# Kernel tuning notes

Measured on AMD Instinct MI355X. Metric: run time of the kernel, lower is better.

Reference implementation:

```python
import jax, jax.numpy as jnp
import numpy as np

EPS = 1e-7
LAMBDA_COORD = 10.0
LAMBDA_NOOBJ = 0.5
LAMBDA_OBJ = 1.0


def setup_inputs() -> dict:
    key = jax.random.key(0)
    k1, k2, k3, k4 = jax.random.split(key, 4)
    B, A, C, G = 64, 3, 20, 76
    predictions = jax.random.normal(k1, (B, A * (5 + C), G, G), dtype=jnp.float32) * 0.5
    txy = jax.random.uniform(k2, (B, A, G, G, 2), dtype=jnp.float32)
    twh = jax.random.normal(k3, (B, A, G, G, 2), dtype=jnp.float32) * 0.3
    tconf = (jax.random.uniform(k4, (B, A, G, G, 1), dtype=jnp.float32) < 0.05).astype(jnp.float32)
    targets = jnp.concatenate([txy, twh, tconf], axis=-1)
    anchors = jnp.array([[1.25, 1.625], [2.0, 3.75], [4.125, 2.875]], dtype=jnp.float32)
    return {"predictions": predictions, "targets": targets, "anchors": anchors}


def _bce(p, t):
    # elementwise binary cross-entropy; p in (0,1) from sigmoid
    return -(t * jnp.log(p) + (1.0 - t) * jnp.log1p(-p))


def _ciou_loss_elem(pb, tb):
    # pb, tb: [..., 4] corner boxes; returns elementwise (1 - ciou)
    x1p, y1p, x2p, y2p = pb[..., 0], pb[..., 1], pb[..., 2], pb[..., 3]
    x1t, y1t, x2t, y2t = tb[..., 0], tb[..., 1], tb[..., 2], tb[..., 3]
    iw = jnp.clip(jnp.minimum(x2p, x2t) - jnp.maximum(x1p, x1t), 0.0)
    ih = jnp.clip(jnp.minimum(y2p, y2t) - jnp.maximum(y1p, y1t), 0.0)
    inter = iw * ih
    area_p = jnp.clip(x2p - x1p, 0.0) * jnp.clip(y2p - y1p, 0.0)
    area_t = jnp.clip(x2t - x1t, 0.0) * jnp.clip(y2t - y1t, 0.0)
    union = area_p + area_t - inter + EPS
    iou = inter / union
    rho2 = ((x1p + x2p - x1t - x2t) * 0.5) ** 2 + ((y1p + y2p - y1t - y2t) * 0.5) ** 2
    en_w = jnp.clip(jnp.maximum(x2p, x2t) - jnp.minimum(x1p, x1t), EPS)
    en_h = jnp.clip(jnp.maximum(y2p, y2t) - jnp.minimum(y1p, y1t), EPS)
    c2 = en_w ** 2 + en_h ** 2
    w_p = jnp.clip(x2p - x1p, EPS); h_p = jnp.clip(y2p - y1p, EPS)
    w_t = jnp.clip(x2t - x1t, EPS); h_t = jnp.clip(y2t - y1t, EPS)
    v = (4.0 / (jnp.pi ** 2)) * (jnp.arctan(w_t / h_t) - jnp.arctan(w_p / h_p)) ** 2
    alpha = jax.lax.stop_gradient(v / (1.0 - iou + v + EPS))
    ciou = iou - rho2 / (c2 + EPS) - alpha * v
    return 1.0 - ciou


def reference(predictions, targets, anchors):
    B, Ch, G, _ = predictions.shape
    A = anchors.shape[0]
    C = Ch // A - 5
    p = predictions.reshape(B, A, 5 + C, G, G).transpose(0, 1, 3, 4, 2)  # [B,A,G,G,5+C]
    pred_xy = jax.nn.sigmoid(p[..., :2])
    pred_wh = p[..., 2:4]
    pred_conf = jax.nn.sigmoid(p[..., 4])
    pred_cls = jax.nn.sigmoid(p[..., 5:])
    obj = targets[..., 4] > 0          # [B,A,G,G]
    n_obj = jnp.sum(obj.astype(jnp.float32))
    n_noobj = jnp.sum((~obj).astype(jnp.float32))
    gy, gx = jnp.meshgrid(jnp.arange(G, dtype=jnp.float32), jnp.arange(G, dtype=jnp.float32), indexing='ij')
    inv_g = 1.0 / G
    aw = anchors[:, 0][None, :, None, None] * inv_g
    ah = anchors[:, 1][None, :, None, None] * inv_g
    # predicted corner boxes
    pcx = (gx + pred_xy[..., 0]) * inv_g
    pcy = (gy + pred_xy[..., 1]) * inv_g
    pw = jnp.exp(pred_wh[..., 0]) * aw
    ph = jnp.exp(pred_wh[..., 1]) * ah
    pred_corners = jnp.clip(jnp.stack([pcx - pw / 2, pcy - ph / 2, pcx + pw / 2, pcy + ph / 2], axis=-1), 0.0, 1.0)
    # target corner boxes
    tcx = (gx + targets[..., 0]) * inv_g
    tcy = (gy + targets[..., 1]) * inv_g
    tw = jnp.exp(targets[..., 2]) * aw
    th = jnp.exp(targets[..., 3]) * ah
    tgt_corners = jnp.clip(jnp.stack([tcx - tw / 2, tcy - th / 2, tcx + tw / 2, tcy + th / 2], axis=-1), 0.0, 1.0)
    ciou_l = _ciou_loss_elem(pred_corners, tgt_corners)  # [B,A,G,G]
    coord_sum = jnp.sum(jnp.where(obj, ciou_l, 0.0))
    coord_loss = jnp.where(n_obj > 0, coord_sum / jnp.maximum(n_obj, 1.0), 0.0)
    conf_bce = _bce(pred_conf, targets[..., 4])
    obj_loss = jnp.where(n_obj > 0, jnp.sum(jnp.where(obj, conf_bce, 0.0)) / jnp.maximum(n_obj, 1.0), 0.0)
    noobj_bce = -jnp.log1p(-pred_conf)  # BCE with target 0
    noobj_loss = jnp.where(n_noobj > 0, jnp.sum(jnp.where(~obj, noobj_bce, 0.0)) / jnp.maximum(n_noobj, 1.0), 0.0)
    if C > 0:
        cls_bce = -jnp.log(pred_cls)  # BCE with target 1
        cls_sum = jnp.sum(jnp.where(obj[..., None], cls_bce, 0.0))
        class_loss = jnp.where(n_obj > 0, cls_sum / jnp.maximum(n_obj * C, 1.0), 0.0)
    else:
        class_loss = jnp.float32(0.0)
    total = LAMBDA_COORD * coord_loss + LAMBDA_OBJ * obj_loss + LAMBDA_NOOBJ * noobj_loss + class_loss
    return total
```

## Files before the change

### kernel.cpp

```cpp
#include <hip/hip_runtime.h>
#include <math.h>

namespace {

constexpr int   kB     = 64;
constexpr int   kA     = 3;
constexpr int   kC     = 20;
constexpr int   kG     = 76;
constexpr int   kGG    = kG * kG;
constexpr int   kCH    = 5 + kC;
constexpr int   kNCell = kB * kA * kGG;
constexpr int   kNC4   = kNCell / 4;
constexpr int   kBlockA = 256;
constexpr int   kGridA  = kNC4 / kBlockA;
constexpr int   kCellsPerBlk = kBlockA * 4;
constexpr float kEps   = 1e-7f;
constexpr float kInvG  = 1.0f / (float)kG;
constexpr float kPiO2  = 1.57079632679f;

constexpr int kPartOff = kGridA;

__device__ __forceinline__ float softplus_fast(float x) {
  return fmaxf(x, 0.0f) + __logf(1.0f + __expf(-fabsf(x)));
}
__device__ __forceinline__ float sigmoidf(float x) {
  return 1.0f / (1.0f + __expf(-x));
}
__device__ __forceinline__ float clamp01(float x) {
  return fminf(fmaxf(x, 0.0f), 1.0f);
}

__device__ __forceinline__ float atan_ratio(float num, float den) {
  const float z  = __fdividef(fminf(num, den), fmaxf(num, den));
  const float z2 = z * z;
  float p = 0.0208351f;
  p = fmaf(p, z2, -0.0851330f);
  p = fmaf(p, z2,  0.1801410f);
  p = fmaf(p, z2, -0.3302995f);
  p = fmaf(p, z2,  0.9998660f);
  const float a = z * p;
  return (num > den) ? (kPiO2 - a) : a;
}

__device__ __forceinline__ void heavy_cell(
    int cell, float tx, float ty, float tw, float th,
    const float* __restrict__ preds, const float* __restrict__ anchors,
    float& coord, float& cls) {
  const int ba = cell / kGG;
  const int j  = cell - ba * kGG;
  const int a  = ba % kA;
  const int gy = j / kG;
  const int gx = j - gy * kG;
  const float fgx = (float)gx, fgy = (float)gy;

  const float aw = anchors[2 * a]     * kInvG;
  const float ah = anchors[2 * a + 1] * kInvG;

  const float* pb = preds + (size_t)ba * kCH * kGG + j;
  const float px  = pb[0];
  const float py  = pb[(size_t)1 * kGG];
  const float pwv = pb[(size_t)2 * kGG];
  const float phv = pb[(size_t)3 * kGG];

  const float pcx = (fgx + sigmoidf(px)) * kInvG;
  const float pcy = (fgy + sigmoidf(py)) * kInvG;
  const float pw  = __expf(pwv) * aw;
  const float ph  = __expf(phv) * ah;
  const float x1p = clamp01(pcx - 0.5f * pw);
  const float y1p = clamp01(pcy - 0.5f * ph);
  const float x2p = clamp01(pcx + 0.5f * pw);
  const float y2p = clamp01(pcy + 0.5f * ph);

  const float tcx = (fgx + tx) * kInvG;
  const float tcy = (fgy + ty) * kInvG;
  const float twv = __expf(tw) * aw;
  const float thv = __expf(th) * ah;
  const float x1t = clamp01(tcx - 0.5f * twv);
  const float y1t = clamp01(tcy - 0.5f * thv);
  const float x2t = clamp01(tcx + 0.5f * twv);
  const float y2t = clamp01(tcy + 0.5f * thv);

  const float iw     = fmaxf(fminf(x2p, x2t) - fmaxf(x1p, x1t), 0.0f);
  const float ih     = fmaxf(fminf(y2p, y2t) - fmaxf(y1p, y1t), 0.0f);
  const float inter  = iw * ih;
  const float area_p = fmaxf(x2p - x1p, 0.0f) * fmaxf(y2p - y1p, 0.0f);
  const float area_t = fmaxf(x2t - x1t, 0.0f) * fmaxf(y2t - y1t, 0.0f);
  const float uni    = area_p + area_t - inter + kEps;
  const float iou    = __fdividef(inter, uni);
  const float dx     = (x1p + x2p - x1t - x2t) * 0.5f;
  const float dy     = (y1p + y2p - y1t - y2t) * 0.5f;
  const float rho2   = dx * dx + dy * dy;
  const float enw    = fmaxf(fmaxf(x2p, x2t) - fminf(x1p, x1t), kEps);
  const float enh    = fmaxf(fmaxf(y2p, y2t) - fminf(y1p, y1t), kEps);
  const float c2     = enw * enw + enh * enh;
  const float wp     = fmaxf(x2p - x1p, kEps);
  const float hp     = fmaxf(y2p - y1p, kEps);
  const float wt     = fmaxf(x2t - x1t, kEps);
  const float ht     = fmaxf(y2t - y1t, kEps);
  const float k4pi2  = 4.0f / (float)(M_PI * M_PI);
  const float dat    = atan_ratio(wt, ht) - atan_ratio(wp, hp);
  const float v      = k4pi2 * dat * dat;
  const float alpha  = __fdividef(v, 1.0f - iou + v + kEps);
  const float ciou   = iou - __fdividef(rho2, c2 + kEps) - alpha * v;
  coord += 1.0f - ciou;

  float cacc = 0.0f;
  #pragma unroll
  for (int c = 0; c < kC; ++c) {
    cacc += softplus_fast(-pb[(size_t)(5 + c) * kGG]);
  }
  cls += cacc;
}

template <int N, int BLK>
__device__ __forceinline__ void block_reduceN(float r[N], float* out) {
  #pragma unroll
  for (int off = 32; off > 0; off >>= 1) {
    #pragma unroll
    for (int s = 0; s < N; ++s) r[s] += __shfl_down(r[s], off, 64);
  }
  __shared__ float red[BLK / 64][N];
  const int lane = threadIdx.x & 63;
  const int wid  = threadIdx.x >> 6;
  if (lane == 0) {
    #pragma unroll
    for (int s = 0; s < N; ++s) red[wid][s] = r[s];
  }
  __syncthreads();
  if (threadIdx.x == 0) {
    #pragma unroll
    for (int s = 0; s < N; ++s) {
      float acc = red[0][s];
      #pragma unroll
      for (int w = 1; w < BLK / 64; ++w) acc += red[w][s];
      out[s] = acc;
    }
  }
}

__global__ __launch_bounds__(kBlockA) void yolo_fused(
    const float* __restrict__ preds,
    const float* __restrict__ tgts,
    const float* __restrict__ anchors,
    int* __restrict__ ws_i) {
  __shared__ int    s_list[kCellsPerBlk];
  __shared__ float4 s_tgt[kCellsPerBlk];
  __shared__ int    s_wtot[kBlockA / 64];

  const int b    = blockIdx.x;
  const int q    = b * kBlockA + threadIdx.x;
  const int cell = q * 4;
  const int ba   = cell / kGG;
  const int j0   = cell - ba * kGG;

  union { float4 v[5]; float f[20]; } T;
  const float4* tb = (const float4*)(tgts + (size_t)cell * 5);
  #pragma unroll
  for (int i = 0; i < 5; ++i) T.v[i] = tb[i];

  const float* p4p = preds + (size_t)ba * kCH * kGG + (size_t)4 * kGG + j0;
  const float4 P4 = *(const float4*)p4p;
  const float p4a[4] = { P4.x, P4.y, P4.z, P4.w };

  float r[4] = {0.f, 0.f, 0.f, 0.f};
  unsigned msk = 0u;

  #pragma unroll
  for (int i = 0; i < 4; ++i) {
    const bool obj = T.f[i * 5 + 4] > 0.0f;
    const float sp = softplus_fast(p4a[i]);
    if (obj) {
      r[0] += sp - p4a[i];
      msk |= (1u << i);
    } else {
      r[1] += sp;
    }
  }
  const int cnt = __popc(msk);

  const int lane = threadIdx.x & 63;
  const int wid  = threadIdx.x >> 6;
  int incl = cnt;
  #pragma unroll
  for (int off = 1; off < 64; off <<= 1) {
    const int n = __shfl_up(incl, off, 64);
    if (lane >= off) incl += n;
  }
  const int excl = incl - cnt;

  if (lane == 63) s_wtot[wid] = incl;
  __syncthreads();

  int wbase = 0;
  #pragma unroll
  for (int w = 0; w < kBlockA / 64; ++w) wbase += (w < wid) ? s_wtot[w] : 0;
  const int total = s_wtot[0] + s_wtot[1] + s_wtot[2] + s_wtot[3];

  if (threadIdx.x == 0) ws_i[b] = total;

  int p = wbase + excl;
  #pragma unroll
  for (int i = 0; i < 4; ++i) {
    if ((msk >> i) & 1u) {
      s_list[p] = cell + i;
      s_tgt[p]  = make_float4(T.f[i * 5 + 0], T.f[i * 5 + 1],
                              T.f[i * 5 + 2], T.f[i * 5 + 3]);
      ++p;
    }
  }
  __syncthreads();

  for (int i = threadIdx.x; i < total; i += kBlockA) {
    const int c  = s_list[i];
    const float4 t4 = s_tgt[i];
    heavy_cell(c, t4.x, t4.y, t4.z, t4.w, preds, anchors, r[2], r[3]);
  }

  block_reduceN<4, kBlockA>(r, (float*)(ws_i + kPartOff) + (size_t)b * 4);
}

__global__ __launch_bounds__(256) void yolo_finish(
    const int* __restrict__ ws_i, float* __restrict__ out) {
  const float* part = (const float*)(ws_i + kPartOff);

  float r[5] = {0.f, 0.f, 0.f, 0.f, 0.f};
  for (int i = threadIdx.x; i < kGridA; i += 256) {
    r[0] += (float)ws_i[i];
    r[1] += part[(size_t)i * 4 + 0];
    r[2] += part[(size_t)i * 4 + 1];
    r[3] += part[(size_t)i * 4 + 2];
    r[4] += part[(size_t)i * 4 + 3];
  }
  __shared__ float outbuf[5];
  block_reduceN<5, 256>(r, outbuf);
  __syncthreads();
  if (threadIdx.x == 0) {
    const float n_obj   = outbuf[0];
    const float objc    = outbuf[1];
    const float noobj   = outbuf[2];
    const float coord   = outbuf[3];
    const float cls     = outbuf[4];
    const float n_noobj = (float)kNCell - n_obj;

    const float coord_loss = (n_obj > 0.f)   ? coord / fmaxf(n_obj, 1.f)   : 0.f;
    const float obj_loss   = (n_obj > 0.f)   ? objc  / fmaxf(n_obj, 1.f)   : 0.f;
    const float noobj_loss = (n_noobj > 0.f) ? noobj / fmaxf(n_noobj, 1.f) : 0.f;
    const float class_loss = (n_obj > 0.f)   ? cls / fmaxf(n_obj * (float)kC, 1.f) : 0.f;

    out[0] = 10.0f * coord_loss + 1.0f * obj_loss + 0.5f * noobj_loss + class_loss;
  }
}

}

extern "C" void kernel_launch(void* const* d_in, const int* in_sizes, int n_in,
                              void* d_out, int out_size, void* d_ws, size_t ws_size,
                              hipStream_t stream) {
  const float* preds   = (const float*)d_in[0];
  const float* tgts    = (const float*)d_in[1];
  const float* anchors = (const float*)d_in[2];
  float* out = (float*)d_out;
  int*   ws  = (int*)d_ws;

  yolo_fused<<<kGridA, kBlockA, 0, stream>>>(preds, tgts, anchors, ws);
  yolo_finish<<<1, 256, 0, stream>>>(ws, out);
}
```

Baseline: 27.05 us.

## Fuse final reduction via last-block atomic counter and split CIoU/class work across waves

Removes the separate finish kernel: each block writes its partials to padded workspace slots, bumps a global atomic counter, and the last block to arrive does the final reduction and writes the loss. The sparse object-cell work is also split so wave 0 computes CIoU while waves 1-3 each handle a slice of the 20 class channels, spreading the gathered class loads across the whole block instead of one thread per cell. A hipMemsetAsync is added to reset the counter each call, and the last block's serial reduction over all partials adds tail latency.

```diff
diff --git a/kernel.cpp b/kernel.cpp
--- a/kernel.cpp
+++ b/kernel.cpp
@@ -3,22 +3,23 @@
 
 namespace {
 
-constexpr int   kB     = 64;
+constexpr int   kBd    = 64;
 constexpr int   kA     = 3;
 constexpr int   kC     = 20;
 constexpr int   kG     = 76;
 constexpr int   kGG    = kG * kG;
 constexpr int   kCH    = 5 + kC;
-constexpr int   kNCell = kB * kA * kGG;
+constexpr int   kNCell = kBd * kA * kGG;
 constexpr int   kNC4   = kNCell / 4;
-constexpr int   kBlockA = 256;
-constexpr int   kGridA  = kNC4 / kBlockA;
-constexpr int   kCellsPerBlk = kBlockA * 4;
+constexpr int   kBlk   = 256;
+constexpr int   kGrid  = kNC4 / kBlk;
+constexpr int   kCellsPerBlk = kBlk * 4;
 constexpr float kEps   = 1e-7f;
 constexpr float kInvG  = 1.0f / (float)kG;
 constexpr float kPiO2  = 1.57079632679f;
 
-constexpr int kPartOff = kGridA;
+constexpr int kPartOff    = 16;
+constexpr int kPartStride = 16;
 
 __device__ __forceinline__ float softplus_fast(float x) {
   return fmaxf(x, 0.0f) + __logf(1.0f + __expf(-fabsf(x)));
@@ -42,10 +43,9 @@
   return (num > den) ? (kPiO2 - a) : a;
 }
 
-__device__ __forceinline__ void heavy_cell(
+__device__ __forceinline__ float ciou_cell(
     int cell, float tx, float ty, float tw, float th,
-    const float* __restrict__ preds, const float* __restrict__ anchors,
-    float& coord, float& cls) {
+    const float* __restrict__ preds, const float* __restrict__ anchors) {
   const int ba = cell / kGG;
   const int j  = cell - ba * kGG;
   const int a  = ba % kA;
@@ -102,24 +102,16 @@
   const float v      = k4pi2 * dat * dat;
   const float alpha  = __fdividef(v, 1.0f - iou + v + kEps);
   const float ciou   = iou - __fdividef(rho2, c2 + kEps) - alpha * v;
-  coord += 1.0f - ciou;
-
-  float cacc = 0.0f;
-  #pragma unroll
-  for (int c = 0; c < kC; ++c) {
-    cacc += softplus_fast(-pb[(size_t)(5 + c) * kGG]);
-  }
-  cls += cacc;
+  return 1.0f - ciou;
 }
 
 template <int N, int BLK>
-__device__ __forceinline__ void block_reduceN(float r[N], float* out) {
+__device__ __forceinline__ void block_reduceN(float r[N], float red[][N], float acc[N]) {
   #pragma unroll
   for (int off = 32; off > 0; off >>= 1) {
     #pragma unroll
     for (int s = 0; s < N; ++s) r[s] += __shfl_down(r[s], off, 64);
   }
-  __shared__ float red[BLK / 64][N];
   const int lane = threadIdx.x & 63;
   const int wid  = threadIdx.x >> 6;
   if (lane == 0) {
@@ -130,25 +122,28 @@
   if (threadIdx.x == 0) {
     #pragma unroll
     for (int s = 0; s < N; ++s) {
-      float acc = red[0][s];
+      float a = red[0][s];
       #pragma unroll
-      for (int w = 1; w < BLK / 64; ++w) acc += red[w][s];
-      out[s] = acc;
-    }
-  }
-}
-
-__global__ __launch_bounds__(kBlockA) void yolo_fused(
+      for (int w = 1; w < BLK / 64; ++w) a += red[w][s];
+      acc[s] = a;
+    }
+  }
+}
+
+__global__ __launch_bounds__(kBlk) void yolo_fused(
     const float* __restrict__ preds,
     const float* __restrict__ tgts,
     const float* __restrict__ anchors,
-    int* __restrict__ ws_i) {
+    uint* __restrict__ ws,
+    float* __restrict__ out) {
   __shared__ int    s_list[kCellsPerBlk];
   __shared__ float4 s_tgt[kCellsPerBlk];
-  __shared__ int    s_wtot[kBlockA / 64];
+  __shared__ int    s_wtot[kBlk / 64];
+  __shared__ float  s_red[kBlk / 64][5];
+  __shared__ int    s_last;
 
   const int b    = blockIdx.x;
-  const int q    = b * kBlockA + threadIdx.x;
+  const int q    = b * kBlk + threadIdx.x;
   const int cell = q * 4;
   const int ba   = cell / kGG;
   const int j0   = cell - ba * kGG;
@@ -162,7 +157,7 @@
   const float4 P4 = *(const float4*)p4p;
   const float p4a[4] = { P4.x, P4.y, P4.z, P4.w };
 
-  float r[4] = {0.f, 0.f, 0.f, 0.f};
+  float r[5] = {0.f, 0.f, 0.f, 0.f, 0.f};
   unsigned msk = 0u;
 
   #pragma unroll
@@ -171,6 +166,7 @@
     const float sp = softplus_fast(p4a[i]);
     if (obj) {
       r[0] += sp - p4a[i];
+      r[4] += 1.0f;
       msk |= (1u << i);
     } else {
       r[1] += sp;
@@ -193,10 +189,8 @@
 
   int wbase = 0;
   #pragma unroll
-  for (int w = 0; w < kBlockA / 64; ++w) wbase += (w < wid) ? s_wtot[w] : 0;
+  for (int w = 0; w < kBlk / 64; ++w) wbase += (w < wid) ? s_wtot[w] : 0;
   const int total = s_wtot[0] + s_wtot[1] + s_wtot[2] + s_wtot[3];
-
-  if (threadIdx.x == 0) ws_i[b] = total;
 
   int p = wbase + excl;
   #pragma unroll
@@ -210,36 +204,61 @@
   }
   __syncthreads();
 
-  for (int i = threadIdx.x; i < total; i += kBlockA) {
-    const int c  = s_list[i];
-    const float4 t4 = s_tgt[i];
-    heavy_cell(c, t4.x, t4.y, t4.z, t4.w, preds, anchors, r[2], r[3]);
-  }
-
-  block_reduceN<4, kBlockA>(r, (float*)(ws_i + kPartOff) + (size_t)b * 4);
-}
-
-__global__ __launch_bounds__(256) void yolo_finish(
-    const int* __restrict__ ws_i, float* __restrict__ out) {
-  const float* part = (const float*)(ws_i + kPartOff);
-
-  float r[5] = {0.f, 0.f, 0.f, 0.f, 0.f};
-  for (int i = threadIdx.x; i < kGridA; i += 256) {
-    r[0] += (float)ws_i[i];
-    r[1] += part[(size_t)i * 4 + 0];
-    r[2] += part[(size_t)i * 4 + 1];
-    r[3] += part[(size_t)i * 4 + 2];
-    r[4] += part[(size_t)i * 4 + 3];
-  }
-  __shared__ float outbuf[5];
-  block_reduceN<5, 256>(r, outbuf);
-  __syncthreads();
+  if (wid == 0) {
+    for (int i = lane; i < total; i += 64) {
+      const float4 t4 = s_tgt[i];
+      r[2] += ciou_cell(s_list[i], t4.x, t4.y, t4.z, t4.w, preds, anchors);
+    }
+  } else {
+    const int c0 = 7 * (wid - 1);
+    const int nc = (wid == 3) ? 6 : 7;
+    for (int i = lane; i < total; i += 64) {
+      const int c   = s_list[i];
+      const int cba = c / kGG;
+      const int cj  = c - cba * kGG;
+      const float* cp = preds + (size_t)cba * kCH * kGG + (size_t)(5 + c0) * kGG + cj;
+      float cacc = 0.0f;
+      #pragma unroll 7
+      for (int k = 0; k < nc; ++k) cacc += softplus_fast(-cp[(size_t)k * kGG]);
+      r[3] += cacc;
+    }
+  }
+
+  float acc[5];
+  block_reduceN<5, kBlk>(r, s_red, acc);
+
   if (threadIdx.x == 0) {
-    const float n_obj   = outbuf[0];
-    const float objc    = outbuf[1];
-    const float noobj   = outbuf[2];
-    const float coord   = outbuf[3];
-    const float cls     = outbuf[4];
+    float* part = (float*)(ws + kPartOff) + (size_t)b * kPartStride;
+    #pragma unroll
+    for (int s = 0; s < 5; ++s)
+      __hip_atomic_store(&part[s], acc[s], __ATOMIC_RELAXED, __HIP_MEMORY_SCOPE_AGENT);
+    __threadfence();
+    const uint old = __hip_atomic_fetch_add(ws, 1u, __ATOMIC_ACQ_REL,
+                                            __HIP_MEMORY_SCOPE_AGENT);
+    s_last = (old == (uint)(kGrid - 1)) ? 1 : 0;
+  }
+  __syncthreads();
+  if (!s_last) return;
+
+  __threadfence();
+  float f[5] = {0.f, 0.f, 0.f, 0.f, 0.f};
+  const float* part = (const float*)(ws + kPartOff);
+  for (int i = threadIdx.x; i < kGrid; i += kBlk) {
+    const float* pi = part + (size_t)i * kPartStride;
+    #pragma unroll
+    for (int s = 0; s < 5; ++s)
+      f[s] += __hip_atomic_load(&pi[s], __ATOMIC_RELAXED, __HIP_MEMORY_SCOPE_AGENT);
+  }
+  __syncthreads();
+  float facc[5];
+  block_reduceN<5, kBlk>(f, s_red, facc);
+
+  if (threadIdx.x == 0) {
+    const float objc    = facc[0];
+    const float noobj   = facc[1];
+    const float coord   = facc[2];
+    const float cls     = facc[3];
+    const float n_obj   = facc[4];
     const float n_noobj = (float)kNCell - n_obj;
 
     const float coord_loss = (n_obj > 0.f)   ? coord / fmaxf(n_obj, 1.f)   : 0.f;
@@ -260,8 +279,8 @@
   const float* tgts    = (const float*)d_in[1];
   const float* anchors = (const float*)d_in[2];
   float* out = (float*)d_out;
-  int*   ws  = (int*)d_ws;
-
-  yolo_fused<<<kGridA, kBlockA, 0, stream>>>(preds, tgts, anchors, ws);
-  yolo_finish<<<1, 256, 0, stream>>>(ws, out);
-}
+  uint*  ws  = (uint*)d_ws;
+
+  hipMemsetAsync(ws, 0, 4, stream);
+  yolo_fused<<<kGrid, kBlk, 0, stream>>>(preds, tgts, anchors, ws, out);
+}
```

Result: slower. 88.74 us (+228.1%).
